# Kernel optimization log

Hardware: AMD Instinct MI355X
Metric: run time of the kernel (lower is better)

Reference implementation:

```python
import jax, jax.numpy as jnp
import numpy as np

B, C, T = 16, 512, 1024      # batch, in_shape (channels), seq_len
H, D = 8, 64                 # num_heads, head_dim; embed = H*D == C
E = H * D
EPS = 1e-6


def setup_inputs() -> dict:
    key = jax.random.key(0)
    ks = jax.random.split(key, 10)
    s_in = 1.0 / np.sqrt(C)
    s_e = 1.0 / np.sqrt(E)
    return {
        "X": jax.random.normal(ks[0], (B, C, T), jnp.float32),
        "ln_g": jnp.ones((C,), jnp.float32),
        "ln_b": jnp.zeros((C,), jnp.float32),
        "Wq": jax.random.normal(ks[1], (C, E), jnp.float32) * s_in,
        "bq": jnp.zeros((E,), jnp.float32),
        "Wk": jax.random.normal(ks[2], (C, E), jnp.float32) * s_in,
        "bk": jnp.zeros((E,), jnp.float32),
        "Wv": jax.random.normal(ks[3], (C, E), jnp.float32) * s_in,
        "bv": jnp.zeros((E,), jnp.float32),
        "Wo": jax.random.normal(ks[4], (E, C), jnp.float32) * s_e,
        "bo": jnp.zeros((C,), jnp.float32),
    }


def reference(X, ln_g, ln_b, Wq, bq, Wk, bk, Wv, bv, Wo, bo):
    # dimshuffle: (B, C, T) -> (B, T, C)
    x = jnp.transpose(X, (0, 2, 1))
    # pre-norm LayerNorm over last dim, eps=1e-6
    mu = jnp.mean(x, axis=-1, keepdims=True)
    var = jnp.mean(jnp.square(x - mu), axis=-1, keepdims=True)
    xn = (x - mu) * jax.lax.rsqrt(var + EPS) * ln_g + ln_b
    # QKV projections, split into heads: (B, T, H, D)
    q = (xn @ Wq + bq).reshape(B, T, H, D)
    k = (xn @ Wk + bk).reshape(B, T, H, D)
    v = (xn @ Wv + bv).reshape(B, T, H, D)
    # attention: scores (B, H, T, T)
    scores = jnp.einsum("bqhd,bkhd->bhqk", q, k) / np.sqrt(D)
    w = jax.nn.softmax(scores, axis=-1)
    h = jnp.einsum("bhqk,bkhd->bqhd", w, v).reshape(B, T, E)
    out = h @ Wo + bo            # output projection (dropout=0 in eval)
    out = x + out                # residual
    return jnp.transpose(out, (0, 2, 1))  # back to (B, C, T)
```

## Files before the change

kernel.cpp:

```cpp
#include <hip/hip_runtime.h>
#include <hip/hip_bf16.h>
#include <cstdint>
#include <cstddef>

typedef __attribute__((ext_vector_type(8))) __bf16 bf16x8;
typedef __attribute__((ext_vector_type(4))) float f32x4;
typedef __attribute__((ext_vector_type(16))) float f32x16;
typedef __attribute__((ext_vector_type(4))) unsigned short u16x4;
typedef __attribute__((ext_vector_type(4))) unsigned int u32x4;
typedef unsigned int u32;

#define NB 16
#define NC 512
#define NT 1024
#define NH 8
#define ND 64
#define NE 512

__device__ __forceinline__ void gld16(void* lds, const void* g) {
  __builtin_amdgcn_global_load_lds(
      (const __attribute__((address_space(1))) u32*)g,
      (__attribute__((address_space(3))) u32*)lds, 16, 0, 0);
}

__device__ __forceinline__ unsigned short f2bf(float f) {
  __bf16 h = (__bf16)f;
  return __builtin_bit_cast(unsigned short, h);
}

__device__ __forceinline__ float ex2(float x) {
  float r; asm("v_exp_f32 %0, %1" : "=v"(r) : "v"(x)); return r;
}

__device__ __forceinline__ void pl32swap(u32& a, u32& b) {
  asm("v_permlane32_swap_b32 %0, %1" : "+v"(a), "+v"(b));
}

__global__ __launch_bounds__(256) void wt_convert4(
    const float* __restrict__ Wq, const float* __restrict__ Wk,
    const float* __restrict__ Wv, const float* __restrict__ Wo,
    __bf16* __restrict__ Wtq, __bf16* __restrict__ Wtk,
    __bf16* __restrict__ Wtv, __bf16* __restrict__ Wto)
{
  __shared__ float tile[32][33];
  const int w = blockIdx.y;
  const float* W = (w == 0) ? Wq : (w == 1) ? Wk : (w == 2) ? Wv : Wo;
  __bf16*     Wt = (w == 0) ? Wtq : (w == 1) ? Wtk : (w == 2) ? Wtv : Wto;
  const int bx = blockIdx.x & 15, by = blockIdx.x >> 4;
  const int r0 = by * 32, c0 = bx * 32;
  const int tx = threadIdx.x & 31, ty = threadIdx.x >> 5;
#pragma unroll
  for (int i = 0; i < 4; i++)
    tile[ty + i * 8][tx] = W[(size_t)(r0 + ty + i * 8) * 512 + c0 + tx];
  __syncthreads();
#pragma unroll
  for (int i = 0; i < 4; i++) {
    const int cc = ty + i * 8;
    Wt[(size_t)(c0 + cc) * 512 + r0 + tx] = (__bf16)tile[tx][cc];
  }
}

__global__ __launch_bounds__(256) void ln_kernel(
    const float* __restrict__ X, const float* __restrict__ gam,
    const float* __restrict__ bet, __bf16* __restrict__ xn)
{
  __shared__ float tile[16][513];
  __shared__ float mu_s[16], rs_s[16];
  const int b  = blockIdx.x >> 6;
  const int t0 = (blockIdx.x & 63) << 4;
  const int tid = threadIdx.x;
  const int tl = tid & 15, c0 = tid >> 4;
  const float* Xb = X + (size_t)b * NC * NT + t0;
  for (int c = c0; c < NC; c += 16)
    tile[tl][c] = Xb[(size_t)c * NT + tl];
  __syncthreads();
  const int row = tid >> 4, sub = tid & 15;
  float s = 0.f, s2 = 0.f;
  for (int c = sub; c < NC; c += 16) { const float v = tile[row][c]; s += v; s2 += v * v; }
  s += __shfl_xor(s, 1);  s2 += __shfl_xor(s2, 1);
  s += __shfl_xor(s, 2);  s2 += __shfl_xor(s2, 2);
  s += __shfl_xor(s, 4);  s2 += __shfl_xor(s2, 4);
  s += __shfl_xor(s, 8);  s2 += __shfl_xor(s2, 8);
  const float mu   = s * (1.f / NC);
  const float var  = s2 * (1.f / NC) - mu * mu;
  const float rstd = rsqrtf(var + 1e-6f);
  if (sub == 0) { mu_s[row] = mu; rs_s[row] = rstd; }
  __syncthreads();
  __bf16* xo = xn + ((size_t)b * NT + t0) * NC;
  for (int i = tid; i < 16 * NC; i += 256) {
    const int r = i >> 9, c = i & (NC - 1);
    xo[(size_t)r * NC + c] = (__bf16)((tile[r][c] - mu_s[r]) * rs_s[r] * gam[c] + bet[c]);
  }
}

__global__ __launch_bounds__(256) void gemm_qkv(
    const __bf16* __restrict__ A, const __bf16* __restrict__ Wt,
    const float* __restrict__ bq, const float* __restrict__ bk, const float* __restrict__ bv,
    __bf16* __restrict__ qb, __bf16* __restrict__ kb, __bf16* __restrict__ vtb)
{
  __shared__ __align__(16) __bf16 lA[128 * 32];
  __shared__ __align__(16) __bf16 lB[128 * 32];
  __shared__ float tb[4][16][17];
  const int tid = threadIdx.x;
  const int wv = tid >> 6, lane = tid & 63;
  const int bid = blockIdx.x;
  const int mchunk = bid / 192, rem = bid % 192;
  const int xcd = rem & 7, loc = rem >> 3;
  const int mt = mchunk * 16 + xcd * 2 + (loc / 12);
  const int nt = loc % 12;
  const int m0 = mt << 7, n0 = nt << 7;
  const int fr = lane & 15, kq = lane >> 4;
  const int wr = wv >> 1, wc = wv & 1;

  const __bf16* Ag0 = A + (size_t)(m0 + (tid >> 2)) * NC + (tid & 3) * 8;
  const __bf16* Ag1 = Ag0 + (size_t)64 * NC;
  const __bf16* Bg0 = Wt + (size_t)(n0 + (tid >> 2)) * NC + (tid & 3) * 8;
  const __bf16* Bg1 = Bg0 + (size_t)64 * NC;
  __bf16* lA0 = lA + wv * 512; __bf16* lA1 = lA + 2048 + wv * 512;
  __bf16* lB0 = lB + wv * 512; __bf16* lB1 = lB + 2048 + wv * 512;

  f32x4 acc[4][4] = {};
  for (int k0 = 0; k0 < NC; k0 += 32) {
    gld16(lA0, Ag0 + k0); gld16(lA1, Ag1 + k0);
    gld16(lB0, Bg0 + k0); gld16(lB1, Bg1 + k0);
    __syncthreads();
    bf16x8 af[4], bfr[4];
#pragma unroll
    for (int i = 0; i < 4; i++) {
      af[i]  = *(const bf16x8*)&lA[(wr * 64 + i * 16 + fr) * 32 + kq * 8];
      bfr[i] = *(const bf16x8*)&lB[(wc * 64 + i * 16 + fr) * 32 + kq * 8];
    }
#pragma unroll
    for (int i = 0; i < 4; i++)
#pragma unroll
      for (int j = 0; j < 4; j++)
        acc[i][j] = __builtin_amdgcn_mfma_f32_16x16x32_bf16(af[i], bfr[j], acc[i][j], 0, 0, 0);
    __syncthreads();
  }

  const int wsel = n0 >> 9;
  const float* bias = (wsel == 0) ? bq : (wsel == 1) ? bk : bv;
  const float qsc = (wsel == 0) ? 0.18033688011112042f : 1.0f;
  if (wsel < 2) {
#pragma unroll
    for (int i = 0; i < 4; i++) {
#pragma unroll
      for (int j = 0; j < 4; j++) {
        const int ng = (n0 & 511) + wc * 64 + j * 16 + fr;
        const int hh = ng >> 6, dd = ng & 63;
        const float bb = bias[ng];
#pragma unroll
        for (int r = 0; r < 4; r++) {
          const int mg = m0 + wr * 64 + i * 16 + kq * 4 + r;
          const int b = mg >> 10, t = mg & 1023;
          const __bf16 h16 = (__bf16)((acc[i][j][r] + bb) * qsc);
          if (wsel == 0) qb[(((size_t)b * NH + hh) * NT + t) * ND + dd] = h16;
          else           kb[(((size_t)b * NH + hh) * NT + t) * ND + dd] = h16;
        }
      }
    }
  } else {
#pragma unroll
    for (int i = 0; i < 4; i++) {
#pragma unroll
      for (int j = 0; j < 4; j++) {
#pragma unroll
        for (int r = 0; r < 4; r++) tb[wv][kq * 4 + r][fr] = acc[i][j][r];
#pragma unroll
        for (int rr = 0; rr < 4; rr++) {
          const int cloc = kq * 4 + rr;
          const int ng = (n0 & 511) + wc * 64 + j * 16 + cloc;
          const int hh = ng >> 6, dd = ng & 63;
          const int mg = m0 + wr * 64 + i * 16 + fr;
          const int b = mg >> 10, t = mg & 1023;
          vtb[(((size_t)b * NH + hh) * ND + dd) * NT + t] =
              (__bf16)(tb[wv][fr][cloc] + bias[ng]);
        }
      }
    }
  }
}

__global__ __launch_bounds__(128, 2) void attn_kernel(
    const __bf16* __restrict__ qb, const __bf16* __restrict__ kb,
    const __bf16* __restrict__ vtb, __bf16* __restrict__ hb)
{
  __shared__ __align__(16) __bf16 lK[2][4096];
  __shared__ __align__(16) __bf16 lV[2][4096];
  const int tid = threadIdx.x, wv = tid >> 6, lane = tid & 63;
  const int l31 = lane & 31, hi = lane >> 5;
  const int swz = (l31 & 7) << 4;
  const int bid = blockIdx.x;
  const int xcd = bid & 7, idx = bid >> 3;
  const int hbp = xcd * 16 + (idx >> 3);
  const int chunk = idx & 7;
  const int b = hbp >> 3, hh = hbp & 7;
  const int q0 = chunk * 128 + wv * 64;

  const __bf16* Q = qb + ((size_t)b * NH + hh) * NT * ND;
  const char* Kc = (const char*)(kb  + ((size_t)b * NH + hh) * NT * ND);
  const char* Vc = (const char*)(vtb + ((size_t)b * NH + hh) * ND * NT);

  bf16x8 qf[2][4];
#pragma unroll
  for (int qs = 0; qs < 2; qs++)
#pragma unroll
    for (int ds = 0; ds < 4; ds++)
      qf[qs][ds] = *(const bf16x8*)&Q[(size_t)(q0 + qs * 32 + l31) * ND + ds * 16 + hi * 8];

  float m_run[2] = {-3e38f, -3e38f};
  float l_run[2] = {0.f, 0.f};
  f32x16 O[2][2] = {};
  const f32x16 zz = {};

  auto stage = [&](int nb, int kt64) {
#pragma unroll
    for (int is = 0; is < 4; is++) {
      const int o  = is * 2048 + wv * 1024 + lane * 16;
      const int rr = o >> 7;
      const int cb = (o & 127) ^ ((rr & 7) << 4);
      gld16((char*)&lK[nb][0] + is * 2048 + wv * 1024,
            Kc + (size_t)(kt64 + rr) * 128 + cb);
      gld16((char*)&lV[nb][0] + is * 2048 + wv * 1024,
            Vc + (size_t)rr * 2048 + (size_t)kt64 * 2 + cb);
    }
  };

  stage(0, 0);
  __syncthreads();

  for (int ti = 0; ti < 16; ti++) {
    const int cur = ti & 1;
    if (ti < 15) stage(cur ^ 1, (ti + 1) * 64);
    const char* Kb = (const char*)&lK[cur][0];
    const char* Vb = (const char*)&lV[cur][0];

    f32x16 st[2][2];
    __builtin_amdgcn_s_setprio(1);
#pragma unroll
    for (int ks = 0; ks < 2; ks++) {
#pragma unroll
      for (int ds = 0; ds < 4; ds++) {
        const int row = ks * 32 + l31;
        const bf16x8 ka = *(const bf16x8*)
            (Kb + row * 128 + ((ds * 32 + hi * 16) ^ swz));
        if (ds == 0) {
          st[0][ks] = __builtin_amdgcn_mfma_f32_32x32x16_bf16(ka, qf[0][0], zz, 0, 0, 0);
          st[1][ks] = __builtin_amdgcn_mfma_f32_32x32x16_bf16(ka, qf[1][0], zz, 0, 0, 0);
        } else {
          st[0][ks] = __builtin_amdgcn_mfma_f32_32x32x16_bf16(ka, qf[0][ds], st[0][ks], 0, 0, 0);
          st[1][ks] = __builtin_amdgcn_mfma_f32_32x32x16_bf16(ka, qf[1][ds], st[1][ks], 0, 0, 0);
        }
      }
    }
    __builtin_amdgcn_s_setprio(0);

#pragma unroll
    for (int qs = 0; qs < 2; qs++) {
      float tm = -3e38f;
#pragma unroll
      for (int ks = 0; ks < 2; ks++)
#pragma unroll
        for (int r = 0; r < 16; r++) tm = fmaxf(tm, st[qs][ks][r]);
      tm = fmaxf(tm, __shfl_xor(tm, 32));
      if (!__all(tm <= m_run[qs] + 8.f)) {
        const float m_new = fmaxf(m_run[qs], tm);
        const float alpha = ex2(m_run[qs] - m_new);
        m_run[qs] = m_new;
        l_run[qs] *= alpha;
        O[qs][0] *= alpha;
        O[qs][1] *= alpha;
      }
      const float mcur = m_run[qs];

      float rs = 0.f;
      u32 pk[2][4][2];
#pragma unroll
      for (int ks = 0; ks < 2; ks++)
#pragma unroll
        for (int g = 0; g < 4; g++) {
          const float p0 = ex2(st[qs][ks][4 * g + 0] - mcur);
          const float p1 = ex2(st[qs][ks][4 * g + 1] - mcur);
          const float p2 = ex2(st[qs][ks][4 * g + 2] - mcur);
          const float p3 = ex2(st[qs][ks][4 * g + 3] - mcur);
          rs += (p0 + p1) + (p2 + p3);
          asm("v_cvt_pk_bf16_f32 %0, %1, %2" : "=v"(pk[ks][g][0]) : "v"(p0), "v"(p1));
          asm("v_cvt_pk_bf16_f32 %0, %1, %2" : "=v"(pk[ks][g][1]) : "v"(p2), "v"(p3));
        }
      rs += __shfl_xor(rs, 32);
      l_run[qs] += rs;

      __builtin_amdgcn_s_setprio(1);
#pragma unroll
      for (int s = 0; s < 4; s++) {
        const int t = s >> 1, m = s & 1;
        u32 a0 = pk[t][2 * m][0], b0 = pk[t][2 * m + 1][0];
        u32 a1 = pk[t][2 * m][1], b1 = pk[t][2 * m + 1][1];
        pl32swap(a0, b0);
        pl32swap(a1, b1);
        u32x4 w;
        w[0] = a0; w[1] = a1; w[2] = b0; w[3] = b1;
        const bf16x8 pfrag = __builtin_bit_cast(bf16x8, w);
#pragma unroll
        for (int dsub = 0; dsub < 2; dsub++) {
          const int row = dsub * 32 + l31;
          const bf16x8 vf = *(const bf16x8*)
              (Vb + row * 128 + ((s * 32 + hi * 16) ^ swz));
          O[qs][dsub] = __builtin_amdgcn_mfma_f32_32x32x16_bf16(vf, pfrag, O[qs][dsub], 0, 0, 0);
        }
      }
      __builtin_amdgcn_s_setprio(0);
    }
    __syncthreads();
  }

#pragma unroll
  for (int qs = 0; qs < 2; qs++) {
    const float linv = 1.f / l_run[qs];
    const int t = q0 + qs * 32 + l31;
    __bf16* hrow = hb + ((size_t)b * NT + t) * NE + hh * ND;
#pragma unroll
    for (int dsub = 0; dsub < 2; dsub++)
#pragma unroll
      for (int g = 0; g < 4; g++) {
        u16x4 ov;
#pragma unroll
        for (int rr = 0; rr < 4; rr++) ov[rr] = f2bf(O[qs][dsub][4 * g + rr] * linv);
        *(u16x4*)&hrow[dsub * 32 + g * 8 + hi * 4] = ov;
      }
  }
}

__global__ __launch_bounds__(256) void gemm_out(
    const __bf16* __restrict__ A, const __bf16* __restrict__ Wt,
    const float* __restrict__ bo, const float* __restrict__ X,
    float* __restrict__ out)
{
  __shared__ __align__(16) __bf16 lA[128 * 32];
  __shared__ __align__(16) __bf16 lB[128 * 32];
  __shared__ float tb[4][16][17];
  const int tid = threadIdx.x, wv = tid >> 6, lane = tid & 63;
  const int bid = blockIdx.x;
  const int mt = ((bid >> 5) << 3) + (bid & 7);
  const int nt = (bid & 31) >> 3;
  const int m0 = mt << 7, n0 = nt << 7;
  const int fr = lane & 15, kq = lane >> 4;
  const int wr = wv >> 1, wc = wv & 1;

  const __bf16* Ag0 = A + (size_t)(m0 + (tid >> 2)) * NE + (tid & 3) * 8;
  const __bf16* Ag1 = Ag0 + (size_t)64 * NE;
  const __bf16* Bg0 = Wt + (size_t)(n0 + (tid >> 2)) * NE + (tid & 3) * 8;
  const __bf16* Bg1 = Bg0 + (size_t)64 * NE;
  __bf16* lA0 = lA + wv * 512; __bf16* lA1 = lA + 2048 + wv * 512;
  __bf16* lB0 = lB + wv * 512; __bf16* lB1 = lB + 2048 + wv * 512;

  f32x4 acc[4][4] = {};
  for (int k0 = 0; k0 < NE; k0 += 32) {
    gld16(lA0, Ag0 + k0); gld16(lA1, Ag1 + k0);
    gld16(lB0, Bg0 + k0); gld16(lB1, Bg1 + k0);
    __syncthreads();
    bf16x8 af[4], bfr[4];
#pragma unroll
    for (int i = 0; i < 4; i++) {
      af[i]  = *(const bf16x8*)&lA[(wr * 64 + i * 16 + fr) * 32 + kq * 8];
      bfr[i] = *(const bf16x8*)&lB[(wc * 64 + i * 16 + fr) * 32 + kq * 8];
    }
#pragma unroll
    for (int i = 0; i < 4; i++)
#pragma unroll
      for (int j = 0; j < 4; j++)
        acc[i][j] = __builtin_amdgcn_mfma_f32_16x16x32_bf16(af[i], bfr[j], acc[i][j], 0, 0, 0);
    __syncthreads();
  }

#pragma unroll
  for (int i = 0; i < 4; i++) {
#pragma unroll
    for (int j = 0; j < 4; j++) {
#pragma unroll
      for (int r = 0; r < 4; r++) tb[wv][kq * 4 + r][fr] = acc[i][j][r];
#pragma unroll
      for (int rr = 0; rr < 4; rr++) {
        const int cloc = kq * 4 + rr;
        const int mg = m0 + wr * 64 + i * 16 + fr;
        const int b = mg >> 10, t = mg & 1023;
        const int c = n0 + wc * 64 + j * 16 + cloc;
        out[((size_t)b * NC + c) * NT + t] =
            tb[wv][fr][cloc] + bo[c] + X[((size_t)b * NC + c) * NT + t];
      }
    }
  }
}

extern "C" void kernel_launch(void* const* d_in, const int* in_sizes, int n_in,
                              void* d_out, int out_size, void* d_ws, size_t ws_size,
                              hipStream_t stream) {
  const float* X   = (const float*)d_in[0];
  const float* lng = (const float*)d_in[1];
  const float* lnb = (const float*)d_in[2];
  const float* Wq  = (const float*)d_in[3];
  const float* bq  = (const float*)d_in[4];
  const float* Wk  = (const float*)d_in[5];
  const float* bk  = (const float*)d_in[6];
  const float* Wv  = (const float*)d_in[7];
  const float* bv  = (const float*)d_in[8];
  const float* Wo  = (const float*)d_in[9];
  const float* bo  = (const float*)d_in[10];
  float* out = (float*)d_out;

  __bf16* wsb   = (__bf16*)d_ws;
  __bf16* Wtqkv = wsb;
  __bf16* Wot   = wsb + 786432;
  __bf16* xn    = wsb + 1048576;
  __bf16* qbuf  = wsb + 9437184;
  __bf16* kbuf  = wsb + 17825792;
  __bf16* vtbuf = wsb + 26214400;
  __bf16* hbuf  = wsb + 34603008;

  wt_convert4<<<dim3(256, 4), 256, 0, stream>>>(
      Wq, Wk, Wv, Wo, Wtqkv, Wtqkv + 262144, Wtqkv + 524288, Wot);
  ln_kernel<<<NB * (NT / 16), 256, 0, stream>>>(X, lng, lnb, xn);
  gemm_qkv<<<128 * 12, 256, 0, stream>>>(xn, Wtqkv, bq, bk, bv, qbuf, kbuf, vtbuf);
  attn_kernel<<<1024, 128, 0, stream>>>(qbuf, kbuf, vtbuf, hbuf);
  gemm_out<<<128 * 4, 256, 0, stream>>>(hbuf, Wot, bo, X, out);
}
```

Baseline: 149.9 us.

## Load attention K/V fragments directly from global memory, dropping LDS staging

The attention kernel no longer double-buffers K and V tiles in shared memory through async global-to-LDS loads. Each wave now reads its MFMA operand fragments straight from global memory into registers and relies on the cache for reuse. The kernel also goes from 2-wave blocks with 1024 blocks to 4-wave blocks with 512 blocks, and the per-tile block barrier is removed. This trades LDS traffic and synchronisation for more global/L2 load traffic, more register pressure, and no explicit prefetch of the next tile.

Measured after the change: 167.1 us. 11.5% more time.

```diff
diff --git a/kernel.cpp b/kernel.cpp
--- a/kernel.cpp
+++ b/kernel.cpp
@@ -181,21 +181,18 @@
   }
 }
 
-__global__ __launch_bounds__(128, 2) void attn_kernel(
+__global__ __launch_bounds__(256) void attn_kernel(
     const __bf16* __restrict__ qb, const __bf16* __restrict__ kb,
     const __bf16* __restrict__ vtb, __bf16* __restrict__ hb)
 {
-  __shared__ __align__(16) __bf16 lK[2][4096];
-  __shared__ __align__(16) __bf16 lV[2][4096];
   const int tid = threadIdx.x, wv = tid >> 6, lane = tid & 63;
   const int l31 = lane & 31, hi = lane >> 5;
-  const int swz = (l31 & 7) << 4;
   const int bid = blockIdx.x;
   const int xcd = bid & 7, idx = bid >> 3;
-  const int hbp = xcd * 16 + (idx >> 3);
-  const int chunk = idx & 7;
+  const int hbp = xcd * 16 + (idx >> 2);
+  const int chunk = idx & 3;
   const int b = hbp >> 3, hh = hbp & 7;
-  const int q0 = chunk * 128 + wv * 64;
+  const int q0 = chunk * 256 + wv * 64;
 
   const __bf16* Q = qb + ((size_t)b * NH + hh) * NT * ND;
   const char* Kc = (const char*)(kb  + ((size_t)b * NH + hh) * NT * ND);
@@ -213,55 +210,43 @@
   f32x16 O[2][2] = {};
   const f32x16 zz = {};
 
-  auto stage = [&](int nb, int kt64) {
-#pragma unroll
-    for (int is = 0; is < 4; is++) {
-      const int o  = is * 2048 + wv * 1024 + lane * 16;
-      const int rr = o >> 7;
-      const int cb = (o & 127) ^ ((rr & 7) << 4);
-      gld16((char*)&lK[nb][0] + is * 2048 + wv * 1024,
-            Kc + (size_t)(kt64 + rr) * 128 + cb);
-      gld16((char*)&lV[nb][0] + is * 2048 + wv * 1024,
-            Vc + (size_t)rr * 2048 + (size_t)kt64 * 2 + cb);
-    }
-  };
-
-  stage(0, 0);
-  __syncthreads();
+  const char* Kl = Kc + (size_t)l31 * 128 + hi * 16;
+  const char* Vl = Vc + (size_t)l31 * 2048 + hi * 16;
 
   for (int ti = 0; ti < 16; ti++) {
-    const int cur = ti & 1;
-    if (ti < 15) stage(cur ^ 1, (ti + 1) * 64);
-    const char* Kb = (const char*)&lK[cur][0];
-    const char* Vb = (const char*)&lV[cur][0];
-
-    f32x16 st[2][2];
-    __builtin_amdgcn_s_setprio(1);
-#pragma unroll
-    for (int ks = 0; ks < 2; ks++) {
-#pragma unroll
-      for (int ds = 0; ds < 4; ds++) {
-        const int row = ks * 32 + l31;
-        const bf16x8 ka = *(const bf16x8*)
-            (Kb + row * 128 + ((ds * 32 + hi * 16) ^ swz));
-        if (ds == 0) {
-          st[0][ks] = __builtin_amdgcn_mfma_f32_32x32x16_bf16(ka, qf[0][0], zz, 0, 0, 0);
-          st[1][ks] = __builtin_amdgcn_mfma_f32_32x32x16_bf16(ka, qf[1][0], zz, 0, 0, 0);
-        } else {
-          st[0][ks] = __builtin_amdgcn_mfma_f32_32x32x16_bf16(ka, qf[0][ds], st[0][ks], 0, 0, 0);
-          st[1][ks] = __builtin_amdgcn_mfma_f32_32x32x16_bf16(ka, qf[1][ds], st[1][ks], 0, 0, 0);
-        }
-      }
-    }
-    __builtin_amdgcn_s_setprio(0);
+    const int kt = ti * 64;
+
+    bf16x8 ka[2][4];
+#pragma unroll
+    for (int ks = 0; ks < 2; ks++)
+#pragma unroll
+      for (int ds = 0; ds < 4; ds++)
+        ka[ks][ds] = *(const bf16x8*)(Kl + (size_t)kt * 128 + ks * 4096 + ds * 32);
+    bf16x8 vf[4][2];
+#pragma unroll
+    for (int s = 0; s < 4; s++)
+#pragma unroll
+      for (int dsub = 0; dsub < 2; dsub++)
+        vf[s][dsub] = *(const bf16x8*)(Vl + (size_t)dsub * 65536 + (size_t)kt * 2 + s * 32);
 
 #pragma unroll
     for (int qs = 0; qs < 2; qs++) {
+      f32x16 st[2];
+      __builtin_amdgcn_s_setprio(1);
+#pragma unroll
+      for (int ks = 0; ks < 2; ks++) {
+        st[ks] = __builtin_amdgcn_mfma_f32_32x32x16_bf16(ka[ks][0], qf[qs][0], zz, 0, 0, 0);
+#pragma unroll
+        for (int ds = 1; ds < 4; ds++)
+          st[ks] = __builtin_amdgcn_mfma_f32_32x32x16_bf16(ka[ks][ds], qf[qs][ds], st[ks], 0, 0, 0);
+      }
+      __builtin_amdgcn_s_setprio(0);
+
       float tm = -3e38f;
 #pragma unroll
       for (int ks = 0; ks < 2; ks++)
 #pragma unroll
-        for (int r = 0; r < 16; r++) tm = fmaxf(tm, st[qs][ks][r]);
+        for (int r = 0; r < 16; r++) tm = fmaxf(tm, st[ks][r]);
       tm = fmaxf(tm, __shfl_xor(tm, 32));
       if (!__all(tm <= m_run[qs] + 8.f)) {
         const float m_new = fmaxf(m_run[qs], tm);
@@ -279,10 +264,10 @@
       for (int ks = 0; ks < 2; ks++)
 #pragma unroll
         for (int g = 0; g < 4; g++) {
-          const float p0 = ex2(st[qs][ks][4 * g + 0] - mcur);
-          const float p1 = ex2(st[qs][ks][4 * g + 1] - mcur);
-          const float p2 = ex2(st[qs][ks][4 * g + 2] - mcur);
-          const float p3 = ex2(st[qs][ks][4 * g + 3] - mcur);
+          const float p0 = ex2(st[ks][4 * g + 0] - mcur);
+          const float p1 = ex2(st[ks][4 * g + 1] - mcur);
+          const float p2 = ex2(st[ks][4 * g + 2] - mcur);
+          const float p3 = ex2(st[ks][4 * g + 3] - mcur);
           rs += (p0 + p1) + (p2 + p3);
           asm("v_cvt_pk_bf16_f32 %0, %1, %2" : "=v"(pk[ks][g][0]) : "v"(p0), "v"(p1));
           asm("v_cvt_pk_bf16_f32 %0, %1, %2" : "=v"(pk[ks][g][1]) : "v"(p2), "v"(p3));
@@ -301,17 +286,11 @@
         u32x4 w;
         w[0] = a0; w[1] = a1; w[2] = b0; w[3] = b1;
         const bf16x8 pfrag = __builtin_bit_cast(bf16x8, w);
-#pragma unroll
-        for (int dsub = 0; dsub < 2; dsub++) {
-          const int row = dsub * 32 + l31;
-          const bf16x8 vf = *(const bf16x8*)
-              (Vb + row * 128 + ((s * 32 + hi * 16) ^ swz));
-          O[qs][dsub] = __builtin_amdgcn_mfma_f32_32x32x16_bf16(vf, pfrag, O[qs][dsub], 0, 0, 0);
-        }
+        O[qs][0] = __builtin_amdgcn_mfma_f32_32x32x16_bf16(vf[s][0], pfrag, O[qs][0], 0, 0, 0);
+        O[qs][1] = __builtin_amdgcn_mfma_f32_32x32x16_bf16(vf[s][1], pfrag, O[qs][1], 0, 0, 0);
       }
       __builtin_amdgcn_s_setprio(0);
     }
-    __syncthreads();
   }
 
 #pragma unroll
@@ -421,6 +400,6 @@
       Wq, Wk, Wv, Wo, Wtqkv, Wtqkv + 262144, Wtqkv + 524288, Wot);
   ln_kernel<<<NB * (NT / 16), 256, 0, stream>>>(X, lng, lnb, xn);
   gemm_qkv<<<128 * 12, 256, 0, stream>>>(xn, Wtqkv, bq, bk, bv, qbuf, kbuf, vtbuf);
-  attn_kernel<<<1024, 128, 0, stream>>>(qbuf, kbuf, vtbuf, hbuf);
+  attn_kernel<<<512, 256, 0, stream>>>(qbuf, kbuf, vtbuf, hbuf);
   gemm_out<<<128 * 4, 256, 0, stream>>>(hbuf, Wot, bo, X, out);
 }
```
